# Kernel tuning notes

Measured on AMD Instinct MI355X. Metric: run time of the kernel, lower is better.

The kernel has to match this reference:

```python
import jax, jax.numpy as jnp
import numpy as np

B = 131072      # batch
NC = 1000       # num_classes
A = 128         # action_dim
ELD = 128       # embedding_latent_dim
VQN = 512       # vq_num_embeddings
VQD = 64        # vq_embedding_dim
SQUISH = 1.0
CC = 0.25       # commitment cost

def _he(k, fi, fo):
    lim = float(np.sqrt(6.0 / fi))
    return jax.random.uniform(k, (fi, fo), jnp.float32, -lim, lim)

def setup_inputs() -> dict:
    key = jax.random.key(0)
    ks = jax.random.split(key, 16)
    cb_lim = float(np.sqrt(3.0 / VQD))  # variance_scaling fan_in uniform
    return {
        "obs": jax.random.randint(ks[0], (B,), 0, NC),
        "embed": jax.random.normal(ks[1], (NC, ELD), jnp.float32) * 0.02,
        "W1": _he(ks[2], ELD, 128), "b1": jnp.zeros((128,), jnp.float32),
        "W2": _he(ks[3], 128, 128), "b2": jnp.zeros((128,), jnp.float32),
        "W3": _he(ks[4], 128, 128), "b3": jnp.zeros((128,), jnp.float32),
        "Wp": _he(ks[5], 128, VQD), "bp": jnp.zeros((VQD,), jnp.float32),
        "codebook": jax.random.uniform(ks[6], (VQN, VQD), jnp.float32, -cb_lim, cb_lim),
        "Wa": jax.random.normal(ks[7], (VQD, A), jnp.float32) * 0.01, "ba": jnp.zeros((A,), jnp.float32),
        "Ws": jax.random.normal(ks[8], (VQD, A), jnp.float32) * 0.01, "bs": jnp.zeros((A,), jnp.float32),
        "Wc1": _he(ks[9], VQD, 128), "bc1": jnp.zeros((128,), jnp.float32),
        "Wc2": _he(ks[10], 128, 128), "bc2": jnp.zeros((128,), jnp.float32),
        "Wc3": _he(ks[11], 128, 32), "bc3": jnp.zeros((32,), jnp.float32),
        "Wc4": _he(ks[12], 32, 1), "bc4": jnp.zeros((1,), jnp.float32),
    }

def reference(obs, embed, W1, b1, W2, b2, W3, b3, Wp, bp, codebook,
              Wa, ba, Ws, bs, Wc1, bc1, Wc2, bc2, Wc3, bc3, Wc4, bc4):
    # embedding lookup + small dense stack
    y = jnp.take(embed, obs, axis=0)                 # [B, 128]
    z = jax.nn.relu(y @ W1 + b1)
    z = jax.nn.relu(z @ W2 + b2)
    z = jax.nn.relu(z @ W3 + b3)
    z = z @ Wp + bp                                  # [B, 64] project to vq dim
    # VQ: pairwise squared distances, argmin, gather (== one_hot @ codebook)
    d = (jnp.sum(z * z, axis=1, keepdims=True)
         - 2.0 * (z @ codebook.T)
         + jnp.sum(codebook * codebook, axis=1))     # [B, 512]
    idx = jnp.argmin(d, axis=1)                      # [B]
    quant = jnp.take(codebook, idx, axis=0)          # [B, 64]
    q = z + jax.lax.stop_gradient(quant - z)         # straight-through
    e_loss = jnp.mean((jax.lax.stop_gradient(q) - z) ** 2)
    q_loss = jnp.mean((q - jax.lax.stop_gradient(z)) ** 2)
    vq_loss = q_loss + CC * e_loss
    # actor heads (pi = MvNormalDiag(actor_mean, scale_diag); return params)
    actor_mean = jax.nn.sigmoid(q @ Wa + ba)
    scale_diag = jax.nn.sigmoid(q @ Ws + bs) * SQUISH + 1e-8
    # critic head
    c = jax.nn.sigmoid(q @ Wc1 + bc1)
    c = jax.nn.sigmoid(c @ Wc2 + bc2)
    c = jax.nn.sigmoid(c @ Wc3 + bc3)
    critic = jnp.squeeze(c @ Wc4 + bc4, axis=-1)     # [B]
    return actor_mean, scale_diag, critic, vq_loss, idx
```

## Files before the change

kernel.cpp:

```cpp
#include <hip/hip_runtime.h>
#include <math.h>


typedef float f4 __attribute__((ext_vector_type(4)));

__device__ __forceinline__ float sigmoidf_(float x){ return 1.0f/(1.0f + expf(-x)); }

__global__ __launch_bounds__(256) void per_class_kernel(
    const float* __restrict__ embed,
    const float* __restrict__ W1, const float* __restrict__ b1,
    const float* __restrict__ W2, const float* __restrict__ b2,
    const float* __restrict__ W3, const float* __restrict__ b3,
    const float* __restrict__ Wp, const float* __restrict__ bp,
    const float* __restrict__ cb,
    const float* __restrict__ Wa, const float* __restrict__ ba,
    const float* __restrict__ Ws, const float* __restrict__ bs,
    const float* __restrict__ Wc1, const float* __restrict__ bc1,
    const float* __restrict__ Wc2, const float* __restrict__ bc2,
    const float* __restrict__ Wc3, const float* __restrict__ bc3,
    const float* __restrict__ Wc4, const float* __restrict__ bc4,
    float* __restrict__ am_t, float* __restrict__ sd_t,
    float* __restrict__ cr_t, int* __restrict__ idx_t, float* __restrict__ e_t,
    float* __restrict__ loss_slot, int VQN)
{
    const int c    = blockIdx.x;
    const int t    = threadIdx.x;
    const int tt   = t & 127;
    const int half = t >> 7;

    if (c == 0 && t == 0) *loss_slot = 0.0f;

    __shared__ double Abuf[128];
    __shared__ double Bbuf[128];
    __shared__ double part[256];
    __shared__ double zp[64];
    __shared__ float  qv[64];
    __shared__ double rd[256];
    __shared__ int    ri[256];
    __shared__ float  h1[128], h2[128], h3[32];

    if (t < 128) Abuf[t] = (double)embed[(size_t)c * 128 + t];
    __syncthreads();

#define LAYER(Xin, Wm, bias, Yout)                                          \
    {                                                                        \
        const int i0 = half * 64;                                            \
        double a0 = 0.0, a1 = 0.0, a2 = 0.0, a3 = 0.0;                       \
        for (int i = 0; i < 64; i += 4) {                                    \
            a0 = fma(Xin[i0+i+0], (double)Wm[(i0+i+0) * 128 + tt], a0);      \
            a1 = fma(Xin[i0+i+1], (double)Wm[(i0+i+1) * 128 + tt], a1);      \
            a2 = fma(Xin[i0+i+2], (double)Wm[(i0+i+2) * 128 + tt], a2);      \
            a3 = fma(Xin[i0+i+3], (double)Wm[(i0+i+3) * 128 + tt], a3);      \
        }                                                                    \
        part[t] = (a0 + a1) + (a2 + a3);                                     \
        __syncthreads();                                                     \
        if (t < 128) {                                                       \
            double acc = (double)bias[t] + part[t] + part[t + 128];          \
            Yout[t] = acc > 0.0 ? acc : 0.0;                                 \
        }                                                                    \
        __syncthreads();                                                     \
    }

    LAYER(Abuf, W1, b1, Bbuf)
    LAYER(Bbuf, W2, b2, Abuf)
    LAYER(Abuf, W3, b3, Bbuf)
#undef LAYER

    {
        const int out = t & 63;
        const int i0  = (t >> 6) * 32;
        double a0 = 0.0, a1 = 0.0, a2 = 0.0, a3 = 0.0;
        for (int i = 0; i < 32; i += 4) {
            a0 = fma(Bbuf[i0+i+0], (double)Wp[(i0+i+0) * 64 + out], a0);
            a1 = fma(Bbuf[i0+i+1], (double)Wp[(i0+i+1) * 64 + out], a1);
            a2 = fma(Bbuf[i0+i+2], (double)Wp[(i0+i+2) * 64 + out], a2);
            a3 = fma(Bbuf[i0+i+3], (double)Wp[(i0+i+3) * 64 + out], a3);
        }
        part[t] = (a0 + a1) + (a2 + a3);
        __syncthreads();
        if (t < 64)
            zp[t] = ((double)bp[t] + part[t] + part[t + 64])
                    + (part[t + 128] + part[t + 192]);
        __syncthreads();
    }

    {
        double best = 1e300; int bidx = 0;
        for (int k = t; k < VQN; k += 256) {
            const float* crow = cb + (size_t)k * 64;
            double s0 = 0.0, s1 = 0.0;
            for (int j = 0; j < 64; j += 2) {
                double d0 = zp[j+0] - (double)crow[j+0];
                double d1 = zp[j+1] - (double)crow[j+1];
                s0 = fma(d0, d0, s0);
                s1 = fma(d1, d1, s1);
            }
            double s = s0 + s1;
            if (s < best) { best = s; bidx = k; }
        }
        rd[t] = best; ri[t] = bidx;
    }
    __syncthreads();
    for (int sft = 128; sft > 0; sft >>= 1) {
        if (t < sft) {
            if (rd[t + sft] < rd[t] || (rd[t + sft] == rd[t] && ri[t + sft] < ri[t])) {
                rd[t] = rd[t + sft]; ri[t] = ri[t + sft];
            }
        }
        __syncthreads();
    }
    const int widx = ri[0];
    if (t < 64) qv[t] = cb[(size_t)widx * 64 + t];
    __syncthreads();

    if (half == 0) {
        float la0 = ba[tt],  la1 = 0.0f;
        float l10 = bc1[tt], l11 = 0.0f;
        for (int j = 0; j < 64; j += 2) {
            float q0 = qv[j], q1 = qv[j+1];
            la0 = fmaf(q0, Wa[j * 128 + tt], la0);
            la1 = fmaf(q1, Wa[(j+1) * 128 + tt], la1);
            l10 = fmaf(q0, Wc1[j * 128 + tt], l10);
            l11 = fmaf(q1, Wc1[(j+1) * 128 + tt], l11);
        }
        am_t[(size_t)c * 128 + tt] = sigmoidf_(la0 + la1);
        h1[tt] = sigmoidf_(l10 + l11);
    } else {
        float ls0 = bs[tt], ls1 = 0.0f;
        for (int j = 0; j < 64; j += 2) {
            ls0 = fmaf(qv[j],   Ws[j * 128 + tt],     ls0);
            ls1 = fmaf(qv[j+1], Ws[(j+1) * 128 + tt], ls1);
        }
        sd_t[(size_t)c * 128 + tt] = sigmoidf_(ls0 + ls1) * 1.0f + 1e-8f;
    }
    __syncthreads();

    if (t < 128) {
        float l20 = bc2[t], l21 = 0.0f;
        for (int i = 0; i < 128; i += 2) {
            l20 = fmaf(h1[i],   Wc2[i * 128 + t],     l20);
            l21 = fmaf(h1[i+1], Wc2[(i+1) * 128 + t], l21);
        }
        h2[t] = sigmoidf_(l20 + l21);
    }
    __syncthreads();

    if (t < 32) {
        float l30 = bc3[t], l31 = 0.0f;
        for (int i = 0; i < 128; i += 2) {
            l30 = fmaf(h2[i],   Wc3[i * 32 + t],     l30);
            l31 = fmaf(h2[i+1], Wc3[(i+1) * 32 + t], l31);
        }
        h3[t] = sigmoidf_(l30 + l31);
    }
    __syncthreads();

    if (t < 32) {
        float p = h3[t] * Wc4[t];
        for (int s = 16; s > 0; s >>= 1) p += __shfl_down(p, s, 64);
        if (t == 0) { cr_t[c] = p + bc4[0]; idx_t[c] = widx; }
    }
    if (t < 64) {
        double d = (double)qv[t] - zp[t];
        double s = d * d;
        for (int sh = 32; sh > 0; sh >>= 1) s += __shfl_down(s, sh, 64);
        if (t == 0) e_t[c] = (float)s;
    }
}

__global__ __launch_bounds__(256) void scatter_vec_kernel(
    const int* __restrict__ obs,
    const f4* __restrict__ am_t, const f4* __restrict__ sd_t,
    const float* __restrict__ cr_t, const int* __restrict__ idx_t,
    f4* __restrict__ out_am, f4* __restrict__ out_sd,
    float* __restrict__ out_critic, float* __restrict__ out_idx, int B)
{
    int gid = blockIdx.x * 256 + threadIdx.x;
    int half = B * 32;
    if (gid < half) {
        int b = gid >> 5;
        int j = gid & 31;
        int o = obs[b];
        __builtin_nontemporal_store(am_t[(size_t)o * 32 + j], &out_am[gid]);
        if (j == 0) __builtin_nontemporal_store(cr_t[o], &out_critic[b]);
    } else {
        int g = gid - half;
        int b = g >> 5;
        int j = g & 31;
        int o = obs[b];
        __builtin_nontemporal_store(sd_t[(size_t)o * 32 + j], &out_sd[g]);
        if (j == 0) __builtin_nontemporal_store((float)idx_t[o], &out_idx[b]);
    }
}

__global__ __launch_bounds__(1024) void loss_kernel(
    const int* __restrict__ obs, const float* __restrict__ e_t,
    float* __restrict__ out_loss, int B, float scale)
{
    int i = blockIdx.x * 1024 + threadIdx.x;
    float e = (i < B) ? e_t[obs[i]] : 0.0f;
    for (int s = 32; s > 0; s >>= 1) e += __shfl_down(e, s, 64);
    __shared__ float w[16];
    int lane = threadIdx.x & 63, wid = threadIdx.x >> 6;
    if (lane == 0) w[wid] = e;
    __syncthreads();
    if (threadIdx.x == 0) {
        float s = 0.0f;
        for (int k = 0; k < 16; ++k) s += w[k];
        atomicAdd(out_loss, s * scale);
    }
}

extern "C" void kernel_launch(void* const* d_in, const int* in_sizes, int n_in,
                              void* d_out, int out_size, void* d_ws, size_t ws_size,
                              hipStream_t stream)
{
    const int*   obs   = (const int*)  d_in[0];
    const float* embed = (const float*)d_in[1];
    const float* W1    = (const float*)d_in[2];
    const float* b1    = (const float*)d_in[3];
    const float* W2    = (const float*)d_in[4];
    const float* b2    = (const float*)d_in[5];
    const float* W3    = (const float*)d_in[6];
    const float* b3    = (const float*)d_in[7];
    const float* Wp    = (const float*)d_in[8];
    const float* bp    = (const float*)d_in[9];
    const float* cb    = (const float*)d_in[10];
    const float* Wa    = (const float*)d_in[11];
    const float* ba    = (const float*)d_in[12];
    const float* Ws    = (const float*)d_in[13];
    const float* bs    = (const float*)d_in[14];
    const float* Wc1   = (const float*)d_in[15];
    const float* bc1   = (const float*)d_in[16];
    const float* Wc2   = (const float*)d_in[17];
    const float* bc2   = (const float*)d_in[18];
    const float* Wc3   = (const float*)d_in[19];
    const float* bc3   = (const float*)d_in[20];
    const float* Wc4   = (const float*)d_in[21];
    const float* bc4   = (const float*)d_in[22];

    const int B   = in_sizes[0];
    const int NC  = in_sizes[1] / 128;
    const int VQN = in_sizes[10] / 64;

    float* am_t = (float*)d_ws;
    float* sd_t = am_t + (size_t)NC * 128;
    float* cr_t = sd_t + (size_t)NC * 128;
    float* e_t  = cr_t + NC;
    int*   idx_t = (int*)(e_t + NC);

    float* out = (float*)d_out;
    const size_t sd_off   = (size_t)B * 128;
    const size_t cr_off   = (size_t)B * 256;
    const size_t loss_off = cr_off + (size_t)B;
    const size_t idx_off  = loss_off + 1;

    per_class_kernel<<<NC, 256, 0, stream>>>(
        embed, W1, b1, W2, b2, W3, b3, Wp, bp, cb,
        Wa, ba, Ws, bs, Wc1, bc1, Wc2, bc2, Wc3, bc3, Wc4, bc4,
        am_t, sd_t, cr_t, idx_t, e_t, out + loss_off, VQN);

    int vec_threads = 2 * B * 32;
    scatter_vec_kernel<<<vec_threads / 256, 256, 0, stream>>>(
        obs, (const f4*)am_t, (const f4*)sd_t, cr_t, idx_t,
        (f4*)out, (f4*)(out + sd_off),
        out + cr_off, out + idx_off, B);

    loss_kernel<<<(B + 1023) / 1024, 1024, 0, stream>>>(
        obs, e_t, out + loss_off, B, 1.25f / ((float)B * 64.0f));
}
```

Measured before the change: 264.7 us.

## Process four classes per block in per-class kernel to reuse weight loads

```diff
diff --git a/kernel.cpp b/kernel.cpp
--- a/kernel.cpp
+++ b/kernel.cpp
@@ -3,6 +3,8 @@
 
 
 typedef float f4 __attribute__((ext_vector_type(4)));
+
+#define CPB 4
 
 __device__ __forceinline__ float sigmoidf_(float x){ return 1.0f/(1.0f + expf(-x)); }
 
@@ -21,150 +23,183 @@
     const float* __restrict__ Wc4, const float* __restrict__ bc4,
     float* __restrict__ am_t, float* __restrict__ sd_t,
     float* __restrict__ cr_t, int* __restrict__ idx_t, float* __restrict__ e_t,
-    float* __restrict__ loss_slot, int VQN)
+    float* __restrict__ loss_slot, int NC, int VQN)
 {
-    const int c    = blockIdx.x;
-    const int t    = threadIdx.x;
-    const int tt   = t & 127;
-    const int half = t >> 7;
-
-    if (c == 0 && t == 0) *loss_slot = 0.0f;
-
-    __shared__ double Abuf[128];
-    __shared__ double Bbuf[128];
-    __shared__ double part[256];
-    __shared__ double zp[64];
-    __shared__ float  qv[64];
-    __shared__ double rd[256];
-    __shared__ int    ri[256];
-    __shared__ float  h1[128], h2[128], h3[32];
-
-    if (t < 128) Abuf[t] = (double)embed[(size_t)c * 128 + t];
-    __syncthreads();
-
-#define LAYER(Xin, Wm, bias, Yout)                                          \
-    {                                                                        \
-        const int i0 = half * 64;                                            \
-        double a0 = 0.0, a1 = 0.0, a2 = 0.0, a3 = 0.0;                       \
-        for (int i = 0; i < 64; i += 4) {                                    \
-            a0 = fma(Xin[i0+i+0], (double)Wm[(i0+i+0) * 128 + tt], a0);      \
-            a1 = fma(Xin[i0+i+1], (double)Wm[(i0+i+1) * 128 + tt], a1);      \
-            a2 = fma(Xin[i0+i+2], (double)Wm[(i0+i+2) * 128 + tt], a2);      \
-            a3 = fma(Xin[i0+i+3], (double)Wm[(i0+i+3) * 128 + tt], a3);      \
-        }                                                                    \
-        part[t] = (a0 + a1) + (a2 + a3);                                     \
-        __syncthreads();                                                     \
-        if (t < 128) {                                                       \
-            double acc = (double)bias[t] + part[t] + part[t + 128];          \
-            Yout[t] = acc > 0.0 ? acc : 0.0;                                 \
-        }                                                                    \
-        __syncthreads();                                                     \
-    }
-
-    LAYER(Abuf, W1, b1, Bbuf)
-    LAYER(Bbuf, W2, b2, Abuf)
-    LAYER(Abuf, W3, b3, Bbuf)
+    const int t  = threadIdx.x;
+    const int c0 = blockIdx.x * CPB;
+    const int n  = t & 127;
+    const int g  = t >> 7;
+
+    if (blockIdx.x == 0 && t == 0) *loss_slot = 0.0f;
+
+    __shared__ double X[CPB][128];
+    __shared__ double Y[CPB][128];
+    __shared__ double zp[CPB][64];
+    __shared__ float  qv[CPB][64];
+    __shared__ float  h1[CPB][128];
+    __shared__ float  h2[CPB][128];
+    __shared__ float  h3[CPB][32];
+    __shared__ double wbest[4][CPB];
+    __shared__ int    wbidx[4][CPB];
+    __shared__ int    widx[CPB];
+
+    for (int e = t; e < CPB * 128; e += 256) {
+        int lc = e >> 7, col = e & 127;
+        int c = c0 + lc;
+        X[lc][col] = (c < NC) ? (double)embed[(size_t)c * 128 + col] : 0.0;
+    }
+    __syncthreads();
+
+    const int lcA = 2 * g, lcB = 2 * g + 1;
+
+#define LAYER(Xin, Wm, bias, Yout)                                         \
+    {                                                                      \
+        double a0 = 0.0, a1 = 0.0, b0 = 0.0, b1_ = 0.0;                    \
+        for (int i = 0; i < 128; i += 2) {                                 \
+            double w0 = (double)Wm[(i + 0) * 128 + n];                     \
+            double w1 = (double)Wm[(i + 1) * 128 + n];                     \
+            a0  = fma(Xin[lcA][i + 0], w0, a0);                            \
+            a1  = fma(Xin[lcA][i + 1], w1, a1);                            \
+            b0  = fma(Xin[lcB][i + 0], w0, b0);                            \
+            b1_ = fma(Xin[lcB][i + 1], w1, b1_);                           \
+        }                                                                  \
+        double accA = (double)bias[n] + a0 + a1;                           \
+        double accB = (double)bias[n] + b0 + b1_;                          \
+        Yout[lcA][n] = accA > 0.0 ? accA : 0.0;                            \
+        Yout[lcB][n] = accB > 0.0 ? accB : 0.0;                            \
+        __syncthreads();                                                   \
+    }
+
+    LAYER(X, W1, b1, Y)
+    LAYER(Y, W2, b2, X)
+    LAYER(X, W3, b3, Y)
 #undef LAYER
 
     {
-        const int out = t & 63;
-        const int i0  = (t >> 6) * 32;
+        const int j = t & 63, lc = t >> 6;
         double a0 = 0.0, a1 = 0.0, a2 = 0.0, a3 = 0.0;
-        for (int i = 0; i < 32; i += 4) {
-            a0 = fma(Bbuf[i0+i+0], (double)Wp[(i0+i+0) * 64 + out], a0);
-            a1 = fma(Bbuf[i0+i+1], (double)Wp[(i0+i+1) * 64 + out], a1);
-            a2 = fma(Bbuf[i0+i+2], (double)Wp[(i0+i+2) * 64 + out], a2);
-            a3 = fma(Bbuf[i0+i+3], (double)Wp[(i0+i+3) * 64 + out], a3);
-        }
-        part[t] = (a0 + a1) + (a2 + a3);
-        __syncthreads();
-        if (t < 64)
-            zp[t] = ((double)bp[t] + part[t] + part[t + 64])
-                    + (part[t + 128] + part[t + 192]);
-        __syncthreads();
-    }
+        for (int i = 0; i < 128; i += 4) {
+            a0 = fma(Y[lc][i + 0], (double)Wp[(i + 0) * 64 + j], a0);
+            a1 = fma(Y[lc][i + 1], (double)Wp[(i + 1) * 64 + j], a1);
+            a2 = fma(Y[lc][i + 2], (double)Wp[(i + 2) * 64 + j], a2);
+            a3 = fma(Y[lc][i + 3], (double)Wp[(i + 3) * 64 + j], a3);
+        }
+        zp[lc][j] = (double)bp[j] + (a0 + a1) + (a2 + a3);
+    }
+    __syncthreads();
+
+    double best[CPB] = {1e300, 1e300, 1e300, 1e300};
+    int    bidx[CPB] = {0, 0, 0, 0};
+    for (int k = t; k < VQN; k += 256) {
+        const f4* crow = (const f4*)(cb + (size_t)k * 64);
+        double dacc[CPB] = {0.0, 0.0, 0.0, 0.0};
+        for (int j4 = 0; j4 < 16; ++j4) {
+            f4 cv = crow[j4];
+            double c0d = (double)cv.x, c1d = (double)cv.y;
+            double c2d = (double)cv.z, c3d = (double)cv.w;
+            int j = j4 * 4;
+#pragma unroll
+            for (int lc = 0; lc < CPB; ++lc) {
+                double e0 = zp[lc][j + 0] - c0d;
+                double e1 = zp[lc][j + 1] - c1d;
+                double e2 = zp[lc][j + 2] - c2d;
+                double e3 = zp[lc][j + 3] - c3d;
+                dacc[lc] = fma(e0, e0, fma(e1, e1, fma(e2, e2, fma(e3, e3, dacc[lc]))));
+            }
+        }
+#pragma unroll
+        for (int lc = 0; lc < CPB; ++lc) {
+            if (dacc[lc] < best[lc]) { best[lc] = dacc[lc]; bidx[lc] = k; }
+        }
+    }
+#pragma unroll
+    for (int lc = 0; lc < CPB; ++lc) {
+        double b = best[lc]; int bi = bidx[lc];
+        for (int s = 32; s > 0; s >>= 1) {
+            double ob = __shfl_down(b, s, 64);
+            int    oi = __shfl_down(bi, s, 64);
+            if (ob < b || (ob == b && oi < bi)) { b = ob; bi = oi; }
+        }
+        if ((t & 63) == 0) { wbest[t >> 6][lc] = b; wbidx[t >> 6][lc] = bi; }
+    }
+    __syncthreads();
+    if (t < CPB) {
+        double b = wbest[0][t]; int bi = wbidx[0][t];
+        for (int w = 1; w < 4; ++w) {
+            if (wbest[w][t] < b || (wbest[w][t] == b && wbidx[w][t] < bi)) {
+                b = wbest[w][t]; bi = wbidx[w][t];
+            }
+        }
+        widx[t] = bi;
+    }
+    __syncthreads();
 
     {
-        double best = 1e300; int bidx = 0;
-        for (int k = t; k < VQN; k += 256) {
-            const float* crow = cb + (size_t)k * 64;
-            double s0 = 0.0, s1 = 0.0;
-            for (int j = 0; j < 64; j += 2) {
-                double d0 = zp[j+0] - (double)crow[j+0];
-                double d1 = zp[j+1] - (double)crow[j+1];
-                s0 = fma(d0, d0, s0);
-                s1 = fma(d1, d1, s1);
-            }
-            double s = s0 + s1;
-            if (s < best) { best = s; bidx = k; }
-        }
-        rd[t] = best; ri[t] = bidx;
-    }
-    __syncthreads();
-    for (int sft = 128; sft > 0; sft >>= 1) {
-        if (t < sft) {
-            if (rd[t + sft] < rd[t] || (rd[t + sft] == rd[t] && ri[t + sft] < ri[t])) {
-                rd[t] = rd[t + sft]; ri[t] = ri[t + sft];
-            }
-        }
-        __syncthreads();
-    }
-    const int widx = ri[0];
-    if (t < 64) qv[t] = cb[(size_t)widx * 64 + t];
-    __syncthreads();
-
-    if (half == 0) {
-        float la0 = ba[tt],  la1 = 0.0f;
-        float l10 = bc1[tt], l11 = 0.0f;
-        for (int j = 0; j < 64; j += 2) {
-            float q0 = qv[j], q1 = qv[j+1];
-            la0 = fmaf(q0, Wa[j * 128 + tt], la0);
-            la1 = fmaf(q1, Wa[(j+1) * 128 + tt], la1);
-            l10 = fmaf(q0, Wc1[j * 128 + tt], l10);
-            l11 = fmaf(q1, Wc1[(j+1) * 128 + tt], l11);
-        }
-        am_t[(size_t)c * 128 + tt] = sigmoidf_(la0 + la1);
-        h1[tt] = sigmoidf_(l10 + l11);
-    } else {
-        float ls0 = bs[tt], ls1 = 0.0f;
-        for (int j = 0; j < 64; j += 2) {
-            ls0 = fmaf(qv[j],   Ws[j * 128 + tt],     ls0);
-            ls1 = fmaf(qv[j+1], Ws[(j+1) * 128 + tt], ls1);
-        }
-        sd_t[(size_t)c * 128 + tt] = sigmoidf_(ls0 + ls1) * 1.0f + 1e-8f;
-    }
-    __syncthreads();
-
-    if (t < 128) {
-        float l20 = bc2[t], l21 = 0.0f;
-        for (int i = 0; i < 128; i += 2) {
-            l20 = fmaf(h1[i],   Wc2[i * 128 + t],     l20);
-            l21 = fmaf(h1[i+1], Wc2[(i+1) * 128 + t], l21);
-        }
-        h2[t] = sigmoidf_(l20 + l21);
-    }
-    __syncthreads();
-
-    if (t < 32) {
-        float l30 = bc3[t], l31 = 0.0f;
-        for (int i = 0; i < 128; i += 2) {
-            l30 = fmaf(h2[i],   Wc3[i * 32 + t],     l30);
-            l31 = fmaf(h2[i+1], Wc3[(i+1) * 32 + t], l31);
-        }
-        h3[t] = sigmoidf_(l30 + l31);
-    }
-    __syncthreads();
-
-    if (t < 32) {
-        float p = h3[t] * Wc4[t];
-        for (int s = 16; s > 0; s >>= 1) p += __shfl_down(p, s, 64);
-        if (t == 0) { cr_t[c] = p + bc4[0]; idx_t[c] = widx; }
-    }
-    if (t < 64) {
-        double d = (double)qv[t] - zp[t];
+        const int j = t & 63, lc = t >> 6;
+        float q = cb[(size_t)widx[lc] * 64 + j];
+        qv[lc][j] = q;
+        double d = (double)q - zp[lc][j];
         double s = d * d;
         for (int sh = 32; sh > 0; sh >>= 1) s += __shfl_down(s, sh, 64);
-        if (t == 0) e_t[c] = (float)s;
+        if (j == 0 && (c0 + lc) < NC) e_t[c0 + lc] = (float)s;
+    }
+    __syncthreads();
+
+    {
+        float laA = ba[n],  laB = ba[n];
+        float lsA = bs[n],  lsB = bs[n];
+        float l1A = bc1[n], l1B = bc1[n];
+        for (int j = 0; j < 64; ++j) {
+            float wa = Wa[j * 128 + n], ws = Ws[j * 128 + n], w1 = Wc1[j * 128 + n];
+            float qA = qv[lcA][j], qB = qv[lcB][j];
+            laA = fmaf(qA, wa, laA); laB = fmaf(qB, wa, laB);
+            lsA = fmaf(qA, ws, lsA); lsB = fmaf(qB, ws, lsB);
+            l1A = fmaf(qA, w1, l1A); l1B = fmaf(qB, w1, l1B);
+        }
+        int cA = c0 + lcA, cB = c0 + lcB;
+        if (cA < NC) {
+            am_t[(size_t)cA * 128 + n] = sigmoidf_(laA);
+            sd_t[(size_t)cA * 128 + n] = sigmoidf_(lsA) * 1.0f + 1e-8f;
+        }
+        if (cB < NC) {
+            am_t[(size_t)cB * 128 + n] = sigmoidf_(laB);
+            sd_t[(size_t)cB * 128 + n] = sigmoidf_(lsB) * 1.0f + 1e-8f;
+        }
+        h1[lcA][n] = sigmoidf_(l1A);
+        h1[lcB][n] = sigmoidf_(l1B);
+    }
+    __syncthreads();
+
+    {
+        float aA = bc2[n], a2A = 0.0f, aB = bc2[n], a2B = 0.0f;
+        for (int i = 0; i < 128; i += 2) {
+            float w0 = Wc2[(i + 0) * 128 + n], w1 = Wc2[(i + 1) * 128 + n];
+            aA  = fmaf(h1[lcA][i + 0], w0, aA);
+            a2A = fmaf(h1[lcA][i + 1], w1, a2A);
+            aB  = fmaf(h1[lcB][i + 0], w0, aB);
+            a2B = fmaf(h1[lcB][i + 1], w1, a2B);
+        }
+        h2[lcA][n] = sigmoidf_(aA + a2A);
+        h2[lcB][n] = sigmoidf_(aB + a2B);
+    }
+    __syncthreads();
+
+    if (t < 128) {
+        int lc = t >> 5, m = t & 31;
+        float a0 = bc3[m], a1 = 0.0f;
+        for (int i = 0; i < 128; i += 2) {
+            a0 = fmaf(h2[lc][i + 0], Wc3[(i + 0) * 32 + m], a0);
+            a1 = fmaf(h2[lc][i + 1], Wc3[(i + 1) * 32 + m], a1);
+        }
+        h3[lc][m] = sigmoidf_(a0 + a1);
+    }
+    __syncthreads();
+
+    if (t < CPB) {
+        float a = bc4[0];
+        for (int i = 0; i < 32; ++i) a = fmaf(h3[t][i], Wc4[i], a);
+        int c = c0 + t;
+        if (c < NC) { cr_t[c] = a; idx_t[c] = widx[t]; }
     }
 }
 
@@ -255,10 +290,10 @@
     const size_t loss_off = cr_off + (size_t)B;
     const size_t idx_off  = loss_off + 1;
 
-    per_class_kernel<<<NC, 256, 0, stream>>>(
+    per_class_kernel<<<(NC + CPB - 1) / CPB, 256, 0, stream>>>(
         embed, W1, b1, W2, b2, W3, b3, Wp, bp, cb,
         Wa, ba, Ws, bs, Wc1, bc1, Wc2, bc2, Wc3, bc3, Wc4, bc4,
-        am_t, sd_t, cr_t, idx_t, e_t, out + loss_off, VQN);
+        am_t, sd_t, cr_t, idx_t, e_t, out + loss_off, NC, VQN);
 
     int vec_threads = 2 * B * 32;
     scatter_vec_kernel<<<vec_threads / 256, 256, 0, stream>>>(
```

Measured after the change: 271.5 us. +2.6%, slower.
